# Performance work log

Hardware: AMD Instinct MI355X
Metric: run time of the kernel (lower is better)

The kernel has to match this reference:

```python
import jax, jax.numpy as jnp
import numpy as np

N = 20000      # nodes
E = 640000     # edges (avg degree 32)
F_X = 256      # node feature dim
F_E = 256      # edge feature dim
D = 2048       # hidden width
D_OUT = 512    # final Linear out_channels
EPS = 1e-5     # torch LayerNorm default eps


def _glorot_like(k, fan_in, fan_out):
    # torch nn.Linear default: U(-1/sqrt(fan_in), 1/sqrt(fan_in))
    lim = (1.0 / fan_in) ** 0.5
    return jax.random.uniform(k, (fan_in, fan_out), minval=-lim, maxval=lim, dtype=jnp.float32)


def setup_inputs() -> dict:
    key = jax.random.key(0)
    ks = jax.random.split(key, 8)
    return {
        "x": jax.random.normal(ks[0], (N, F_X), dtype=jnp.float32),
        "edge_index": jax.random.randint(ks[1], (2, E), 0, N),
        "edge_attr": jax.random.normal(ks[2], (E, F_E), dtype=jnp.float32),
        # u = (u, nb, eb) in the original; unused by this setup (no conv1d/GraphNorm)
        "u_counts": jnp.array([N], dtype=jnp.int32),
        "nb": jnp.zeros((N,), dtype=jnp.int32),
        "eb": jnp.zeros((E,), dtype=jnp.int32),
        # learned params per setup
        "W1": _glorot_like(ks[3], F_X + F_E, D), "b1": jnp.zeros((D,), jnp.float32),
        "W3": _glorot_like(ks[4], D, D),         "b3": jnp.zeros((D,), jnp.float32),
        "ln_g": jnp.ones((D,), jnp.float32),      "ln_b": jnp.zeros((D,), jnp.float32),
        "W6": _glorot_like(ks[5], D + F_X + F_E, D), "b6": jnp.zeros((D,), jnp.float32),
        "W8": _glorot_like(ks[6], D, D_OUT),      "b8": jnp.zeros((D_OUT,), jnp.float32),
    }


def reference(x, edge_index, edge_attr, u_counts, nb, eb,
              W1, b1, W3, b3, ln_g, ln_b, W6, b6, W8, b8):
    # scatter_mean(edge_attr, col, dim=0, dim_size=N)
    col = edge_index[1]
    seg_sum = jax.ops.segment_sum(edge_attr, col, num_segments=N)           # [N, F_E]
    cnt = jax.ops.segment_sum(jnp.ones((edge_attr.shape[0],), edge_attr.dtype),
                              col, num_segments=N)                           # [N]
    agg = seg_sum / jnp.maximum(cnt, 1.0)[:, None]                           # mean; 0 for empty slots

    h0 = jnp.concatenate([agg, x], axis=1)                                   # [N, F_E+F_X]
    # layer 1-2: Linear -> ReLU
    h2 = jax.nn.relu(h0 @ W1 + b1)                                           # [N, D]
    # layer 3-4: Linear -> ReLU
    h4 = jax.nn.relu(h2 @ W3 + b3)                                           # [N, D]
    # layer 5: LayerNorm (affine)
    mu = jnp.mean(h4, axis=-1, keepdims=True)
    var = jnp.var(h4, axis=-1, keepdims=True)
    h5 = (h4 - mu) * jax.lax.rsqrt(var + EPS) * ln_g + ln_b
    # layer 6-7: Linear over concat(h5, merge_in) -> ReLU  (skip connection)
    h7 = jax.nn.relu(jnp.concatenate([h5, h0], axis=1) @ W6 + b6)            # [N, D]
    # layer 8: Linear -> out[-1]
    return h7 @ W8 + b8                                                      # [N, D_OUT]
```

## Files before the change

kernel.cpp:

```cpp
#include <hip/hip_runtime.h>

typedef unsigned short ushort_t;
typedef __attribute__((ext_vector_type(4))) float f32x4;
typedef __attribute__((ext_vector_type(8))) __bf16 bf16x8;
typedef __attribute__((ext_vector_type(8))) unsigned short u16x8;
typedef __attribute__((ext_vector_type(4))) unsigned short u16x4;

__device__ __forceinline__ unsigned short f2bf(float f) {
  union { float f; unsigned int u; } v; v.f = f;
  unsigned int u = v.u;
  u += 0x7fffu + ((u >> 16) & 1u);
  return (unsigned short)(u >> 16);
}

__device__ __forceinline__ void gload16(ushort_t* lds, const ushort_t* g) {
  __builtin_amdgcn_global_load_lds(
      (const __attribute__((address_space(1))) unsigned int*)g,
      (__attribute__((address_space(3))) unsigned int*)lds, 16, 0, 0);
}

__global__ __launch_bounds__(256)
void transpose_w(const float* __restrict__ in, ushort_t* __restrict__ out, int R, int C) {
  __shared__ float tile[32][33];
  const int t = threadIdx.x;
  const int tx = t & 31, ty = t >> 5;
  const int r0 = blockIdx.x * 32, c0 = blockIdx.y * 32;
#pragma unroll
  for (int i = 0; i < 4; ++i)
    tile[ty + 8 * i][tx] = in[(size_t)(r0 + ty + 8 * i) * C + c0 + tx];
  __syncthreads();
#pragma unroll
  for (int i = 0; i < 4; ++i)
    out[(size_t)(c0 + ty + 8 * i) * R + r0 + tx] = f2bf(tile[tx][ty + 8 * i]);
}

__global__ __launch_bounds__(256)
void count_edges(const int* __restrict__ col, int* __restrict__ cnt, int E) {
  int i = blockIdx.x * 256 + threadIdx.x;
  if (i < E) atomicAdd(&cnt[col[i]], 1);
}

__global__ __launch_bounds__(1024)
void prefix_kernel(const int* __restrict__ cnt, int* __restrict__ start,
                   int* __restrict__ cursor, int N) {
  __shared__ int buf[1024];
  __shared__ int carry_s;
  if (threadIdx.x == 0) carry_s = 0;
  __syncthreads();
  for (int base = 0; base < N; base += 1024) {
    int i = base + threadIdx.x;
    int v = (i < N) ? cnt[i] : 0;
    buf[threadIdx.x] = v;
    __syncthreads();
    for (int off = 1; off < 1024; off <<= 1) {
      int tv = (threadIdx.x >= off) ? buf[threadIdx.x - off] : 0;
      __syncthreads();
      buf[threadIdx.x] += tv;
      __syncthreads();
    }
    int excl = carry_s + buf[threadIdx.x] - v;
    if (i < N) { start[i] = excl; cursor[i] = excl; }
    __syncthreads();
    if (threadIdx.x == 1023) carry_s += buf[1023];
    __syncthreads();
  }
}

__global__ __launch_bounds__(256)
void fill_csr(const int* __restrict__ col, int* __restrict__ cursor,
              int* __restrict__ eids, int E) {
  int i = blockIdx.x * 256 + threadIdx.x;
  if (i < E) {
    int p = atomicAdd(&cursor[col[i]], 1);
    eids[p] = i;
  }
}

__global__ __launch_bounds__(256)
void gather_mean(const float* __restrict__ eattr, const int* __restrict__ start,
                 const int* __restrict__ deg, const int* __restrict__ eids,
                 const float* __restrict__ x, ushort_t* __restrict__ hcat, int N) {
  const int row = blockIdx.x;
  const int t = threadIdx.x;
  const int s = start[row], d = deg[row];
  float sum = 0.f;
  int i = 0;
  for (; i + 4 <= d; i += 4) {
    int e0 = eids[s + i], e1 = eids[s + i + 1], e2 = eids[s + i + 2], e3 = eids[s + i + 3];
    float v0 = eattr[(size_t)e0 * 256 + t];
    float v1 = eattr[(size_t)e1 * 256 + t];
    float v2 = eattr[(size_t)e2 * 256 + t];
    float v3 = eattr[(size_t)e3 * 256 + t];
    sum += v0 + v1 + v2 + v3;
  }
  for (; i < d; ++i) sum += eattr[(size_t)eids[s + i] * 256 + t];
  const float mean = sum / fmaxf((float)d, 1.f);
  hcat[(size_t)row * 2560 + 2048 + t] = f2bf(mean);
  hcat[(size_t)row * 2560 + 2304 + t] = f2bf(x[(size_t)row * 256 + t]);
}

__global__ __launch_bounds__(256)
void ln_kernel(const float* __restrict__ h4, const float* __restrict__ g,
               const float* __restrict__ b, ushort_t* __restrict__ hcat) {
  const int row = blockIdx.x;
  const int t = threadIdx.x;
  const float* p = h4 + (size_t)row * 2048;
  float4 v0 = *(const float4*)(p + t * 8);
  float4 v1 = *(const float4*)(p + t * 8 + 4);
  float vv[8] = {v0.x, v0.y, v0.z, v0.w, v1.x, v1.y, v1.z, v1.w};
  float s = 0.f, ss = 0.f;
#pragma unroll
  for (int j = 0; j < 8; ++j) { s += vv[j]; ss += vv[j] * vv[j]; }
#pragma unroll
  for (int o = 32; o > 0; o >>= 1) {
    s += __shfl_xor(s, o);
    ss += __shfl_xor(ss, o);
  }
  __shared__ float red[8];
  int w = t >> 6, l = t & 63;
  if (l == 0) { red[w] = s; red[4 + w] = ss; }
  __syncthreads();
  s = red[0] + red[1] + red[2] + red[3];
  ss = red[4] + red[5] + red[6] + red[7];
  const float mu = s * (1.f / 2048.f);
  const float var = ss * (1.f / 2048.f) - mu * mu;
  const float rs = rsqrtf(var + 1e-5f);
  float4 g0 = *(const float4*)(g + t * 8);
  float4 g1 = *(const float4*)(g + t * 8 + 4);
  float4 b0 = *(const float4*)(b + t * 8);
  float4 b1 = *(const float4*)(b + t * 8 + 4);
  float gg[8] = {g0.x, g0.y, g0.z, g0.w, g1.x, g1.y, g1.z, g1.w};
  float bb[8] = {b0.x, b0.y, b0.z, b0.w, b1.x, b1.y, b1.z, b1.w};
  u16x8 o8;
#pragma unroll
  for (int j = 0; j < 8; ++j) o8[j] = f2bf((vv[j] - mu) * rs * gg[j] + bb[j]);
  *(u16x8*)(hcat + (size_t)row * 2560 + t * 8) = o8;
}


__device__ __forceinline__ void read_a4(bf16x8 (&dst)[4][2], const char* sb, int bufoff,
                                        int aoff, int slot0, int slot1, int g) {
#pragma unroll
  for (int m = 0; m < 4; ++m) {
    const char* p = sb + bufoff + aoff + (g * 4 + m) * 2048;
    dst[m][0] = *(const bf16x8*)(p + slot0);
    dst[m][1] = *(const bf16x8*)(p + slot1);
  }
}

__device__ __forceinline__ void read_b2(bf16x8 (&dst)[2][2], const char* sb, int bufoff,
                                        int boff, int slot0, int slot1, int g) {
#pragma unroll
  for (int n = 0; n < 2; ++n) {
    const char* p = sb + bufoff + boff + (g * 2 + n) * 2048;
    dst[n][0] = *(const bf16x8*)(p + slot0);
    dst[n][1] = *(const bf16x8*)(p + slot1);
  }
}

__device__ __forceinline__ void mfma_q(f32x4 (&acc)[8][4], const bf16x8 (&a)[4][2],
                                       const bf16x8 (&b)[2][2], int mg, int ng) {
#pragma unroll
  for (int m = 0; m < 4; ++m)
#pragma unroll
    for (int n = 0; n < 2; ++n)
#pragma unroll
      for (int kk = 0; kk < 2; ++kk)
        acc[mg * 4 + m][ng * 2 + n] = __builtin_amdgcn_mfma_f32_16x16x32_bf16(
            a[m][kk], b[n][kk], acc[mg * 4 + m][ng * 2 + n], 0, 0, 0);
}

#define SBAR() do { __builtin_amdgcn_sched_barrier(0); \
                    __builtin_amdgcn_s_barrier(); \
                    __builtin_amdgcn_sched_barrier(0); } while (0)

template <int RELU, int OUTBF>
__global__ __launch_bounds__(512, 2)
void gemm256(const ushort_t* __restrict__ A, int lda,
             const ushort_t* __restrict__ Bt,
             const float* __restrict__ bias,
             void* __restrict__ Cout, int ldc, int M, int K) {
  __shared__ __align__(16) ushort_t smem[65536];
  char* sb = (char*)smem;
  const int t = threadIdx.x;

  const int nct = gridDim.x;
  const int nwg = nct * gridDim.y;
  const int flat = blockIdx.y * nct + blockIdx.x;
  const int xcd = flat & 7, loc = flat >> 3;
  const int q = nwg >> 3, r = nwg & 7;
  const int swz = (xcd < r ? xcd * (q + 1) : r * (q + 1) + (xcd - r) * q) + loc;
  const int row0 = (swz / nct) * 256;
  const int col0 = (swz % nct) * 256;

  const int wid = t >> 6, l = t & 63;
  const int wr = wid >> 2, wc = wid & 3;
  const int lr = l & 15, lk = l >> 4;

  const int srow = t >> 3;
  const int scol = ((t & 7) ^ ((t >> 3) & 7)) << 3;
  const ushort_t* pa[2][2];
  const ushort_t* pb[2][2];
#pragma unroll
  for (int h = 0; h < 2; ++h)
#pragma unroll
    for (int L = 0; L < 2; ++L) {
      int ra = row0 + h * 128 + L * 64 + srow;
      if (ra > M - 1) ra = M - 1;
      pa[h][L] = A + (size_t)ra * lda + scol;
      pb[h][L] = Bt + (size_t)(col0 + h * 128 + L * 64 + srow) * K + scol;
    }
  const int tb = t * 16;

  const int slot0 = ((lk ^ (lr & 7)) << 4);
  const int slot1 = (((4 + lk) ^ (lr & 7)) << 4);
  const int aoff = (wr * 128 + lr) * 128;
  const int boff = 32768 + (wc * 64 + lr) * 128;

  f32x4 acc[8][4] = {};
  bf16x8 af[4][2], af2[4][2], bf[2][2], bf2[2][2];

  const int nk = K >> 6;

  {
    gload16((ushort_t*)(sb + 0 + tb), pa[0][0]);
    gload16((ushort_t*)(sb + 8192 + tb), pa[0][1]);
    gload16((ushort_t*)(sb + 16384 + tb), pa[1][0]);
    gload16((ushort_t*)(sb + 24576 + tb), pa[1][1]);
    gload16((ushort_t*)(sb + 32768 + tb), pb[0][0]);
    gload16((ushort_t*)(sb + 40960 + tb), pb[0][1]);
    gload16((ushort_t*)(sb + 49152 + tb), pb[1][0]);
    gload16((ushort_t*)(sb + 57344 + tb), pb[1][1]);
    const int k1 = (nk > 1) ? 1 : 0;
    gload16((ushort_t*)(sb + 65536 + 32768 + tb), pb[0][0] + (k1 << 6));
    gload16((ushort_t*)(sb + 65536 + 40960 + tb), pb[0][1] + (k1 << 6));
    gload16((ushort_t*)(sb + 65536 + 0 + tb), pa[0][0] + (k1 << 6));
    gload16((ushort_t*)(sb + 65536 + 8192 + tb), pa[0][1] + (k1 << 6));
  }
  asm volatile("s_waitcnt vmcnt(4)" ::: "memory");
  SBAR();

  for (int k = 0; k < nk; ++k) {
    const int cur = (k & 1) << 16, nxt = cur ^ 65536;
    const int kc1 = ((k + 1 < nk) ? k + 1 : nk - 1) << 6;
    const int kc2 = ((k + 2 < nk) ? k + 2 : nk - 1) << 6;

    read_a4(af, sb, cur, aoff, slot0, slot1, 0);
    read_b2(bf, sb, cur, boff, slot0, slot1, 0);
    gload16((ushort_t*)(sb + nxt + 16384 + tb), pa[1][0] + kc1);
    gload16((ushort_t*)(sb + nxt + 24576 + tb), pa[1][1] + kc1);
    SBAR();
    __builtin_amdgcn_s_setprio(1);
    mfma_q(acc, af, bf, 0, 0);
    __builtin_amdgcn_s_setprio(0);
    SBAR();

    read_b2(bf2, sb, cur, boff, slot0, slot1, 1);
    gload16((ushort_t*)(sb + nxt + 49152 + tb), pb[1][0] + kc1);
    gload16((ushort_t*)(sb + nxt + 57344 + tb), pb[1][1] + kc1);
    SBAR();
    __builtin_amdgcn_s_setprio(1);
    mfma_q(acc, af, bf2, 0, 1);
    __builtin_amdgcn_s_setprio(0);
    SBAR();

    read_a4(af2, sb, cur, aoff, slot0, slot1, 1);
    gload16((ushort_t*)(sb + cur + 32768 + tb), pb[0][0] + kc2);
    gload16((ushort_t*)(sb + cur + 40960 + tb), pb[0][1] + kc2);
    SBAR();
    __builtin_amdgcn_s_setprio(1);
    mfma_q(acc, af2, bf, 1, 0);
    __builtin_amdgcn_s_setprio(0);
    SBAR();

    gload16((ushort_t*)(sb + cur + 0 + tb), pa[0][0] + kc2);
    gload16((ushort_t*)(sb + cur + 8192 + tb), pa[0][1] + kc2);
    asm volatile("s_waitcnt vmcnt(4)" ::: "memory");
    SBAR();
    __builtin_amdgcn_s_setprio(1);
    mfma_q(acc, af2, bf2, 1, 1);
    __builtin_amdgcn_s_setprio(0);
    SBAR();
  }

#pragma unroll
  for (int nj = 0; nj < 4; ++nj) {
    const int ocol = col0 + wc * 64 + nj * 16 + lr;
    const float bv = bias[ocol];
#pragma unroll
    for (int mi = 0; mi < 8; ++mi) {
      const int orow = row0 + wr * 128 + mi * 16 + lk * 4;
      f32x4 v = acc[mi][nj];
#pragma unroll
      for (int r2 = 0; r2 < 4; ++r2) {
        if (orow + r2 < M) {
          float o = v[r2] + bv;
          if (RELU) o = fmaxf(o, 0.f);
          if (OUTBF)
            ((ushort_t*)Cout)[(size_t)(orow + r2) * ldc + ocol] = f2bf(o);
          else
            ((float*)Cout)[(size_t)(orow + r2) * ldc + ocol] = o;
        }
      }
    }
  }
}

template <int RELU, int OUTBF>
__global__ __launch_bounds__(256)
void gemm_bt(const ushort_t* __restrict__ A, int lda,
             const ushort_t* __restrict__ Bt,
             const float* __restrict__ bias,
             void* __restrict__ Cout, int ldc, int M, int K) {
  __shared__ __align__(16) ushort_t sA[128 * 32];
  __shared__ __align__(16) ushort_t sB[128 * 32];
  const int t = threadIdx.x;

  const int nct = gridDim.x;
  const int nwg = nct * gridDim.y;
  const int flat = blockIdx.y * nct + blockIdx.x;
  const int xcd = flat & 7, loc = flat >> 3;
  const int q = nwg >> 3, r = nwg & 7;
  const int swz = (xcd < r ? xcd * (q + 1) : r * (q + 1) + (xcd - r) * q) + loc;
  const int row0 = (swz / nct) * 128;
  const int col0 = (swz % nct) * 128;

  const int w = t >> 6, l = t & 63;
  const int wr = (w >> 1) * 64, wc = (w & 1) * 64;
  const int lr = l & 15, lk = l >> 4;

  const int sr = t >> 2;
  const int sk = (t & 3) * 8;
  int ar1 = row0 + sr;       if (ar1 > M - 1) ar1 = M - 1;
  int ar2 = row0 + 64 + sr;  if (ar2 > M - 1) ar2 = M - 1;
  const ushort_t* pa1 = A + (size_t)ar1 * lda + sk;
  const ushort_t* pa2 = A + (size_t)ar2 * lda + sk;
  const ushort_t* pb1 = Bt + (size_t)(col0 + sr) * K + sk;
  const ushort_t* pb2 = Bt + (size_t)(col0 + 64 + sr) * K + sk;
  ushort_t* la1 = sA + 8 * t;
  ushort_t* la2 = sA + 8 * t + 2048;
  ushort_t* lb1 = sB + 8 * t;
  ushort_t* lb2 = sB + 8 * t + 2048;

  f32x4 acc[4][4] = {};

  const int nk = K >> 5;
  for (int kt = 0; kt < nk; ++kt) {
    const int k0 = kt << 5;
    gload16(la1, pa1 + k0);
    gload16(la2, pa2 + k0);
    gload16(lb1, pb1 + k0);
    gload16(lb2, pb2 + k0);
    __syncthreads();
    bf16x8 af[4], bfr[4];
#pragma unroll
    for (int m = 0; m < 4; ++m)
      af[m] = *(const bf16x8*)&sA[(wr + m * 16 + lr) * 32 + lk * 8];
#pragma unroll
    for (int n = 0; n < 4; ++n)
      bfr[n] = *(const bf16x8*)&sB[(wc + n * 16 + lr) * 32 + lk * 8];
#pragma unroll
    for (int m = 0; m < 4; ++m)
#pragma unroll
      for (int n = 0; n < 4; ++n)
        acc[m][n] = __builtin_amdgcn_mfma_f32_16x16x32_bf16(af[m], bfr[n], acc[m][n], 0, 0, 0);
    __syncthreads();
  }

#pragma unroll
  for (int n = 0; n < 4; ++n) {
    const int ocol = col0 + wc + n * 16 + lr;
    const float bv = bias[ocol];
#pragma unroll
    for (int m = 0; m < 4; ++m) {
      const int orow = row0 + wr + m * 16 + lk * 4;
      f32x4 v = acc[m][n];
#pragma unroll
      for (int r2 = 0; r2 < 4; ++r2) {
        if (orow + r2 < M) {
          float o = v[r2] + bv;
          if (RELU) o = fmaxf(o, 0.f);
          if (OUTBF)
            ((ushort_t*)Cout)[(size_t)(orow + r2) * ldc + ocol] = f2bf(o);
          else
            ((float*)Cout)[(size_t)(orow + r2) * ldc + ocol] = o;
        }
      }
    }
  }
}

extern "C" void kernel_launch(void* const* d_in, const int* in_sizes, int n_in,
                              void* d_out, int out_size, void* d_ws, size_t ws_size,
                              hipStream_t stream) {
  (void)n_in; (void)out_size; (void)ws_size;
  const float* x     = (const float*)d_in[0];
  const int*   eidx  = (const int*)d_in[1];
  const float* eattr = (const float*)d_in[2];
  const float* W1 = (const float*)d_in[6];
  const float* b1 = (const float*)d_in[7];
  const float* W3 = (const float*)d_in[8];
  const float* b3 = (const float*)d_in[9];
  const float* lng = (const float*)d_in[10];
  const float* lnb = (const float*)d_in[11];
  const float* W6 = (const float*)d_in[12];
  const float* b6 = (const float*)d_in[13];
  const float* W8 = (const float*)d_in[14];
  const float* b8 = (const float*)d_in[15];

  const int N = in_sizes[0] / 256;
  const int E = in_sizes[2] / 256;
  const int* col = eidx + E;

  char* ws = (char*)d_ws;
  float* h4  = (float*)ws;
  size_t off = (size_t)N * 2048 * 4;
  ushort_t* hcat = (ushort_t*)(ws + off);  off += (size_t)N * 2560 * 2;
  ushort_t* h2   = (ushort_t*)(ws + off);  off += (size_t)N * 2048 * 2;
  ushort_t* W1t = (ushort_t*)(ws + off);   off += (size_t)2048 * 512 * 2;
  ushort_t* W3t = (ushort_t*)(ws + off);   off += (size_t)2048 * 2048 * 2;
  ushort_t* W6t = (ushort_t*)(ws + off);   off += (size_t)2048 * 2560 * 2;
  ushort_t* W8t = (ushort_t*)(ws + off);   off += (size_t)512 * 2048 * 2;
  int* deg    = (int*)(ws + off);  off += (size_t)N * 4;
  int* startp = (int*)(ws + off);  off += (size_t)N * 4;
  int* cursor = (int*)(ws + off);  off += (size_t)N * 4;
  int* eids   = (int*)(ws + off);  off += (size_t)E * 4;

  hipMemsetAsync(deg, 0, (size_t)N * 4, stream);

  transpose_w<<<dim3(512 / 32, 2048 / 32), 256, 0, stream>>>(W1, W1t, 512, 2048);
  transpose_w<<<dim3(2048 / 32, 2048 / 32), 256, 0, stream>>>(W3, W3t, 2048, 2048);
  transpose_w<<<dim3(2560 / 32, 2048 / 32), 256, 0, stream>>>(W6, W6t, 2560, 2048);
  transpose_w<<<dim3(2048 / 32, 512 / 32), 256, 0, stream>>>(W8, W8t, 2048, 512);

  count_edges<<<(E + 255) / 256, 256, 0, stream>>>(col, deg, E);
  prefix_kernel<<<1, 1024, 0, stream>>>(deg, startp, cursor, N);
  fill_csr<<<(E + 255) / 256, 256, 0, stream>>>(col, cursor, eids, E);
  gather_mean<<<N, 256, 0, stream>>>(eattr, startp, deg, eids, x, hcat, N);

  const int Mt256 = (N + 255) / 256;
  const int Mt128 = (N + 127) / 128;
  gemm256<1, 1><<<dim3(8, Mt256), 512, 0, stream>>>(hcat + 2048, 2560, W1t, b1, h2, 2048, N, 512);
  gemm256<1, 0><<<dim3(8, Mt256), 512, 0, stream>>>(h2, 2048, W3t, b3, h4, 2048, N, 2048);
  ln_kernel<<<N, 256, 0, stream>>>(h4, lng, lnb, hcat);
  gemm256<1, 1><<<dim3(8, Mt256), 512, 0, stream>>>(hcat, 2560, W6t, b6, h2, 2048, N, 2560);
  gemm_bt<0, 0><<<dim3(4, Mt128), 256, 0, stream>>>(h2, 2048, W8t, b8, (float*)d_out, 512, N, 2048);
}
```

Baseline: 954.3 us.

## Store h4 as bf16 in place, vectorize gather, parallelize scan, unify final GEMM

The W3 GEMM now writes bf16 output straight into the concat buffer, and LayerNorm runs in place on it. This removes the fp32 h4 round trip through memory, at the cost of computing LayerNorm statistics from bf16-rounded values. The edge gather uses float4 loads split across four waves and reduces through shared memory. The prefix scan becomes a chunked wave-shuffle scan, and the final projection uses the 256-tile GEMM instead of the removed 128-tile kernel, which leaves only 2 column tiles.

```diff
diff --git a/kernel.cpp b/kernel.cpp
--- a/kernel.cpp
+++ b/kernel.cpp
@@ -13,6 +13,11 @@
   return (unsigned short)(u >> 16);
 }
 
+__device__ __forceinline__ float bf2f(unsigned short h) {
+  union { unsigned int u; float f; } v; v.u = ((unsigned int)h) << 16;
+  return v.f;
+}
+
 __device__ __forceinline__ void gload16(ushort_t* lds, const ushort_t* g) {
   __builtin_amdgcn_global_load_lds(
       (const __attribute__((address_space(1))) unsigned int*)g,
@@ -43,26 +48,37 @@
 __global__ __launch_bounds__(1024)
 void prefix_kernel(const int* __restrict__ cnt, int* __restrict__ start,
                    int* __restrict__ cursor, int N) {
-  __shared__ int buf[1024];
-  __shared__ int carry_s;
-  if (threadIdx.x == 0) carry_s = 0;
-  __syncthreads();
-  for (int base = 0; base < N; base += 1024) {
-    int i = base + threadIdx.x;
-    int v = (i < N) ? cnt[i] : 0;
-    buf[threadIdx.x] = v;
-    __syncthreads();
-    for (int off = 1; off < 1024; off <<= 1) {
-      int tv = (threadIdx.x >= off) ? buf[threadIdx.x - off] : 0;
-      __syncthreads();
-      buf[threadIdx.x] += tv;
-      __syncthreads();
+  const int t = threadIdx.x;
+  const int chunk = (N + 1023) >> 10;
+  const int base = t * chunk;
+  int s = 0;
+  for (int j = 0; j < chunk; ++j) {
+    int i = base + j;
+    s += (i < N) ? cnt[i] : 0;
+  }
+  const int lane = t & 63, wv = t >> 6;
+  int scan = s;
+#pragma unroll
+  for (int o = 1; o < 64; o <<= 1) {
+    int up = __shfl_up(scan, o);
+    if (lane >= o) scan += up;
+  }
+  __shared__ int wsum[16];
+  if (lane == 63) wsum[wv] = scan;
+  __syncthreads();
+  if (t == 0) {
+    int acc = 0;
+#pragma unroll
+    for (int i2 = 0; i2 < 16; ++i2) { int v = wsum[i2]; wsum[i2] = acc; acc += v; }
+  }
+  __syncthreads();
+  int run = wsum[wv] + (scan - s);
+  for (int j = 0; j < chunk; ++j) {
+    int i = base + j;
+    if (i < N) {
+      start[i] = run; cursor[i] = run;
+      run += cnt[i];
     }
-    int excl = carry_s + buf[threadIdx.x] - v;
-    if (i < N) { start[i] = excl; cursor[i] = excl; }
-    __syncthreads();
-    if (threadIdx.x == 1023) carry_s += buf[1023];
-    __syncthreads();
   }
 }
 
@@ -82,32 +98,41 @@
                  const float* __restrict__ x, ushort_t* __restrict__ hcat, int N) {
   const int row = blockIdx.x;
   const int t = threadIdx.x;
+  const int w = t >> 6, l = t & 63;
   const int s = start[row], d = deg[row];
-  float sum = 0.f;
-  int i = 0;
-  for (; i + 4 <= d; i += 4) {
-    int e0 = eids[s + i], e1 = eids[s + i + 1], e2 = eids[s + i + 2], e3 = eids[s + i + 3];
-    float v0 = eattr[(size_t)e0 * 256 + t];
-    float v1 = eattr[(size_t)e1 * 256 + t];
-    float v2 = eattr[(size_t)e2 * 256 + t];
-    float v3 = eattr[(size_t)e3 * 256 + t];
-    sum += v0 + v1 + v2 + v3;
-  }
-  for (; i < d; ++i) sum += eattr[(size_t)eids[s + i] * 256 + t];
-  const float mean = sum / fmaxf((float)d, 1.f);
-  hcat[(size_t)row * 2560 + 2048 + t] = f2bf(mean);
+  const float4* ea4 = (const float4*)eattr;
+  float4 sum = make_float4(0.f, 0.f, 0.f, 0.f);
+  for (int i = w; i < d; i += 4) {
+    int e = eids[s + i];
+    float4 v = ea4[(size_t)e * 64 + l];
+    sum.x += v.x; sum.y += v.y; sum.z += v.z; sum.w += v.w;
+  }
+  __shared__ float4 part[4][64];
+  part[w][l] = sum;
+  __syncthreads();
   hcat[(size_t)row * 2560 + 2304 + t] = f2bf(x[(size_t)row * 256 + t]);
-}
-
-__global__ __launch_bounds__(256)
-void ln_kernel(const float* __restrict__ h4, const float* __restrict__ g,
-               const float* __restrict__ b, ushort_t* __restrict__ hcat) {
+  if (w == 0) {
+    float4 a = part[0][l], b = part[1][l], c = part[2][l], dd = part[3][l];
+    const float inv = 1.f / fmaxf((float)d, 1.f);
+    u16x4 o;
+    o[0] = f2bf((a.x + b.x + c.x + dd.x) * inv);
+    o[1] = f2bf((a.y + b.y + c.y + dd.y) * inv);
+    o[2] = f2bf((a.z + b.z + c.z + dd.z) * inv);
+    o[3] = f2bf((a.w + b.w + c.w + dd.w) * inv);
+    *(u16x4*)(hcat + (size_t)row * 2560 + 2048 + l * 4) = o;
+  }
+}
+
+__global__ __launch_bounds__(256)
+void ln_kernel(ushort_t* __restrict__ hcat, const float* __restrict__ g,
+               const float* __restrict__ b) {
   const int row = blockIdx.x;
   const int t = threadIdx.x;
-  const float* p = h4 + (size_t)row * 2048;
-  float4 v0 = *(const float4*)(p + t * 8);
-  float4 v1 = *(const float4*)(p + t * 8 + 4);
-  float vv[8] = {v0.x, v0.y, v0.z, v0.w, v1.x, v1.y, v1.z, v1.w};
+  ushort_t* p = hcat + (size_t)row * 2560 + t * 8;
+  u16x8 raw = *(const u16x8*)p;
+  float vv[8];
+#pragma unroll
+  for (int j = 0; j < 8; ++j) vv[j] = bf2f(raw[j]);
   float s = 0.f, ss = 0.f;
 #pragma unroll
   for (int j = 0; j < 8; ++j) { s += vv[j]; ss += vv[j] * vv[j]; }
@@ -134,7 +159,7 @@
   u16x8 o8;
 #pragma unroll
   for (int j = 0; j < 8; ++j) o8[j] = f2bf((vv[j] - mu) * rs * gg[j] + bb[j]);
-  *(u16x8*)(hcat + (size_t)row * 2560 + t * 8) = o8;
+  *(u16x8*)p = o8;
 }
 
 
@@ -291,90 +316,6 @@
     for (int mi = 0; mi < 8; ++mi) {
       const int orow = row0 + wr * 128 + mi * 16 + lk * 4;
       f32x4 v = acc[mi][nj];
-#pragma unroll
-      for (int r2 = 0; r2 < 4; ++r2) {
-        if (orow + r2 < M) {
-          float o = v[r2] + bv;
-          if (RELU) o = fmaxf(o, 0.f);
-          if (OUTBF)
-            ((ushort_t*)Cout)[(size_t)(orow + r2) * ldc + ocol] = f2bf(o);
-          else
-            ((float*)Cout)[(size_t)(orow + r2) * ldc + ocol] = o;
-        }
-      }
-    }
-  }
-}
-
-template <int RELU, int OUTBF>
-__global__ __launch_bounds__(256)
-void gemm_bt(const ushort_t* __restrict__ A, int lda,
-             const ushort_t* __restrict__ Bt,
-             const float* __restrict__ bias,
-             void* __restrict__ Cout, int ldc, int M, int K) {
-  __shared__ __align__(16) ushort_t sA[128 * 32];
-  __shared__ __align__(16) ushort_t sB[128 * 32];
-  const int t = threadIdx.x;
-
-  const int nct = gridDim.x;
-  const int nwg = nct * gridDim.y;
-  const int flat = blockIdx.y * nct + blockIdx.x;
-  const int xcd = flat & 7, loc = flat >> 3;
-  const int q = nwg >> 3, r = nwg & 7;
-  const int swz = (xcd < r ? xcd * (q + 1) : r * (q + 1) + (xcd - r) * q) + loc;
-  const int row0 = (swz / nct) * 128;
-  const int col0 = (swz % nct) * 128;
-
-  const int w = t >> 6, l = t & 63;
-  const int wr = (w >> 1) * 64, wc = (w & 1) * 64;
-  const int lr = l & 15, lk = l >> 4;
-
-  const int sr = t >> 2;
-  const int sk = (t & 3) * 8;
-  int ar1 = row0 + sr;       if (ar1 > M - 1) ar1 = M - 1;
-  int ar2 = row0 + 64 + sr;  if (ar2 > M - 1) ar2 = M - 1;
-  const ushort_t* pa1 = A + (size_t)ar1 * lda + sk;
-  const ushort_t* pa2 = A + (size_t)ar2 * lda + sk;
-  const ushort_t* pb1 = Bt + (size_t)(col0 + sr) * K + sk;
-  const ushort_t* pb2 = Bt + (size_t)(col0 + 64 + sr) * K + sk;
-  ushort_t* la1 = sA + 8 * t;
-  ushort_t* la2 = sA + 8 * t + 2048;
-  ushort_t* lb1 = sB + 8 * t;
-  ushort_t* lb2 = sB + 8 * t + 2048;
-
-  f32x4 acc[4][4] = {};
-
-  const int nk = K >> 5;
-  for (int kt = 0; kt < nk; ++kt) {
-    const int k0 = kt << 5;
-    gload16(la1, pa1 + k0);
-    gload16(la2, pa2 + k0);
-    gload16(lb1, pb1 + k0);
-    gload16(lb2, pb2 + k0);
-    __syncthreads();
-    bf16x8 af[4], bfr[4];
-#pragma unroll
-    for (int m = 0; m < 4; ++m)
-      af[m] = *(const bf16x8*)&sA[(wr + m * 16 + lr) * 32 + lk * 8];
-#pragma unroll
-    for (int n = 0; n < 4; ++n)
-      bfr[n] = *(const bf16x8*)&sB[(wc + n * 16 + lr) * 32 + lk * 8];
-#pragma unroll
-    for (int m = 0; m < 4; ++m)
-#pragma unroll
-      for (int n = 0; n < 4; ++n)
-        acc[m][n] = __builtin_amdgcn_mfma_f32_16x16x32_bf16(af[m], bfr[n], acc[m][n], 0, 0, 0);
-    __syncthreads();
-  }
-
-#pragma unroll
-  for (int n = 0; n < 4; ++n) {
-    const int ocol = col0 + wc + n * 16 + lr;
-    const float bv = bias[ocol];
-#pragma unroll
-    for (int m = 0; m < 4; ++m) {
-      const int orow = row0 + wr + m * 16 + lk * 4;
-      f32x4 v = acc[m][n];
 #pragma unroll
       for (int r2 = 0; r2 < 4; ++r2) {
         if (orow + r2 < M) {
@@ -413,8 +354,7 @@
   const int* col = eidx + E;
 
   char* ws = (char*)d_ws;
-  float* h4  = (float*)ws;
-  size_t off = (size_t)N * 2048 * 4;
+  size_t off = 0;
   ushort_t* hcat = (ushort_t*)(ws + off);  off += (size_t)N * 2560 * 2;
   ushort_t* h2   = (ushort_t*)(ws + off);  off += (size_t)N * 2048 * 2;
   ushort_t* W1t = (ushort_t*)(ws + off);   off += (size_t)2048 * 512 * 2;
@@ -439,10 +379,9 @@
   gather_mean<<<N, 256, 0, stream>>>(eattr, startp, deg, eids, x, hcat, N);
 
   const int Mt256 = (N + 255) / 256;
-  const int Mt128 = (N + 127) / 128;
   gemm256<1, 1><<<dim3(8, Mt256), 512, 0, stream>>>(hcat + 2048, 2560, W1t, b1, h2, 2048, N, 512);
-  gemm256<1, 0><<<dim3(8, Mt256), 512, 0, stream>>>(h2, 2048, W3t, b3, h4, 2048, N, 2048);
-  ln_kernel<<<N, 256, 0, stream>>>(h4, lng, lnb, hcat);
+  gemm256<1, 1><<<dim3(8, Mt256), 512, 0, stream>>>(h2, 2048, W3t, b3, hcat, 2560, N, 2048);
+  ln_kernel<<<N, 256, 0, stream>>>(hcat, lng, lnb);
   gemm256<1, 1><<<dim3(8, Mt256), 512, 0, stream>>>(hcat, 2560, W6t, b6, h2, 2048, N, 2560);
-  gemm_bt<0, 0><<<dim3(4, Mt128), 256, 0, stream>>>(h2, 2048, W8t, b8, (float*)d_out, 512, N, 2048);
-}
+  gemm256<0, 0><<<dim3(2, Mt256), 512, 0, stream>>>(h2, 2048, W8t, b8, (float*)d_out, 512, N, 2048);
+}
```

Result: faster. 932.7 us (-2.3%).
